# Kernel optimization log

Measured on AMD Instinct MI355X. Metric: run time of the kernel, lower is better.

Reference implementation:

```python
import jax, jax.numpy as jnp
import numpy as np

HID = 512
VOCAB = 2048
K_CB = 4


def conv1d(x, w, b, stride):
    # x: [B, C_in, L], w: [C_out, C_in, 7], torch Conv1d(k=7, stride, pad=3)
    y = jax.lax.conv_general_dilated(
        x, w, window_strides=(stride,), padding=[(3, 3)],
        dimension_numbers=("NCH", "OIH", "NCH"))
    return y + b[None, :, None]


def setup_inputs() -> dict:
    key = jax.random.key(0)
    ks = jax.random.split(key, 9)
    B, S = 4, 32768
    audio = jax.random.normal(ks[0], (B, 1, S), dtype=jnp.float32)
    # encoder params (fan-in scaled init, like torch default scale-wise)
    w1 = jax.random.normal(ks[1], (HID // 4, 1, 7), dtype=jnp.float32) * (1.0 / np.sqrt(1 * 7))
    b1 = jnp.zeros((HID // 4,), dtype=jnp.float32)
    w2 = jax.random.normal(ks[2], (HID // 2, HID // 4, 7), dtype=jnp.float32) * (1.0 / np.sqrt(HID // 4 * 7))
    b2 = jnp.zeros((HID // 2,), dtype=jnp.float32)
    w3 = jax.random.normal(ks[3], (HID, HID // 2, 7), dtype=jnp.float32) * (1.0 / np.sqrt(HID // 2 * 7))
    b3 = jnp.zeros((HID,), dtype=jnp.float32)
    codebook = jax.random.normal(ks[4], (K_CB, VOCAB, HID), dtype=jnp.float32)
    embedding = jax.random.normal(ks[5], (VOCAB, HID), dtype=jnp.float32)
    return {"audio": audio, "w1": w1, "b1": b1, "w2": w2, "b2": b2,
            "w3": w3, "b3": b3, "codebook": codebook, "embedding": embedding}


def reference(audio, w1, b1, w2, b2, w3, b3, codebook, embedding):
    # conv encoder: [B,1,S] -> [B,H,L], L = S/8
    f = jax.nn.relu(conv1d(audio, w1, b1, 2))
    f = jax.nn.relu(conv1d(f, w2, b2, 2))
    f = conv1d(f, w3, b3, 2)
    feats = jnp.transpose(f, (0, 2, 1))  # [B, L, H]

    # multi-codebook nearest neighbor: argmin of squared L2 == argmin of cdist
    f2 = jnp.sum(feats * feats, axis=-1)          # [B, L]
    c2 = jnp.sum(codebook * codebook, axis=-1)    # [K, V]
    cross = jnp.einsum("blh,kvh->bklv", feats, codebook)  # [B, K, L, V]
    d2 = f2[:, None, :, None] + c2[None, :, None, :] - 2.0 * cross
    tokens = jnp.argmin(d2, axis=-1)              # [B, K, L] (stack over codebooks at dim=1)
    emb = embedding[tokens].mean(axis=1)          # [B, L, H]
    return tokens, emb
```

## Files before the change

kernel.cpp:

```cpp
#include <hip/hip_runtime.h>
#include <hip/hip_bf16.h>
#include <stdint.h>

#define B_ 4
#define S_IN 32768
#define C1V 128
#define L1V 16384
#define C2V 256
#define L2V 8192
#define C3V 512
#define L3V 4096
#define VOCABV 2048
#define KCB 4

#define R1P (2 * (L1V + 16))
#define P1P (L1V + 16)
#define R2P (2 * (L2V + 16))
#define P2P (L2V + 16)

typedef _Float16 half8 __attribute__((ext_vector_type(8)));
typedef float floatx4 __attribute__((ext_vector_type(4)));

#define AS1 __attribute__((address_space(1)))
#define AS3 __attribute__((address_space(3)))

__device__ __forceinline__ void gload_lds16(const void* g, void* l) {
    __builtin_amdgcn_global_load_lds((const AS1 void*)g, (AS3 void*)l, 16, 0, 0);
}

__device__ __forceinline__ half8 lds_read_half8_a4(const _Float16* p) {
    union { uint32_t u[4]; half8 h; } t;
    const uint32_t* w = (const uint32_t*)p;
    t.u[0] = w[0]; t.u[1] = w[1]; t.u[2] = w[2]; t.u[3] = w[3];
    return t.h;
}

__global__ void padzero_kernel(_Float16* __restrict__ x1h, _Float16* __restrict__ x2h) {
    int j = blockIdx.x * 256 + threadIdx.x;
    half8 z;
#pragma unroll
    for (int i = 0; i < 8; ++i) z[i] = (_Float16)0.f;
    if (j < 2048) {
        int row = j >> 2, p = j & 3;
        size_t base = (size_t)row * R1P + (size_t)(p >> 1) * P1P + ((p & 1) ? (L1V + 8) : 0);
        *(half8*)(x1h + base) = z;
    } else if (j < 6144) {
        int j2 = j - 2048;
        int row = j2 >> 2, p = j2 & 3;
        size_t base = (size_t)row * R2P + (size_t)(p >> 1) * P2P + ((p & 1) ? (L2V + 8) : 0);
        *(half8*)(x2h + base) = z;
    }
}

__global__ void conv1_kernel(const float* __restrict__ x, const float* __restrict__ w,
                             const float* __restrict__ bias, _Float16* __restrict__ out) {
    __shared__ float xs[2 * 256 + 6];
    __shared__ float ws[7];
    const int l0 = blockIdx.x * 256;
    const int co = blockIdx.y;
    const int b  = blockIdx.z;
    const int tid = threadIdx.x;
    const float* xb = x + (size_t)b * S_IN;
    for (int n = tid; n < 2 * 256 + 6; n += 256) {
        int p = 2 * l0 - 3 + n;
        xs[n] = (p >= 0 && p < S_IN) ? xb[p] : 0.f;
    }
    if (tid < 7) ws[tid] = w[co * 7 + tid];
    __syncthreads();
    float acc = bias[co];
    const int base = 2 * tid;
#pragma unroll
    for (int t = 0; t < 7; ++t) acc = fmaf(ws[t], xs[base + t], acc);
    float s = fmaxf(acc, 0.f) * 1024.f;
    _Float16 h  = (_Float16)s;
    _Float16 lo = (_Float16)(s - (float)h);
    size_t o = (size_t)(b * C1V + co) * R1P + 8 + l0 + tid;
    out[o] = h;
    out[o + P1P] = lo;
}

__global__ void wsplit_kernel(const float* __restrict__ w, _Float16* __restrict__ wh,
                              _Float16* __restrict__ wl, int cin, int cout) {
    int idx = blockIdx.x * 256 + threadIdx.x;
    if (idx >= cin * cout) return;
    int co = idx / cin;
    int ci = idx - co * cin;
    const float* src = w + ((size_t)co * cin + ci) * 7;
    half8 h, l;
    h[0] = (_Float16)0.f; l[0] = (_Float16)0.f;
#pragma unroll
    for (int u = 1; u < 8; ++u) {
        float v = src[u - 1] * 1024.f;
        _Float16 hh = (_Float16)v;
        h[u] = hh;
        l[u] = (_Float16)(v - (float)hh);
    }
    size_t o = (size_t)co * (cin * 8) + ci * 8;
    *(half8*)(wh + o) = h;
    *(half8*)(wl + o) = l;
}


__global__ __launch_bounds__(256, 2) void conv2_mfma_kernel(
    const _Float16* __restrict__ xin, const _Float16* __restrict__ WH,
    const _Float16* __restrict__ WL, const float* __restrict__ bias,
    _Float16* __restrict__ xout) {
    __shared__ _Float16 Xs[2176];
    __shared__ _Float16 WsH[128 * 32], WsL[128 * 32];
    const int tid = threadIdx.x;
    const int wave = tid >> 6;
    const int lane = tid & 63;
    const int wm = wave >> 1, wn = wave & 1;
    const int q  = lane >> 4;
    const int cl = lane & 15;
    const int l0  = blockIdx.x * 128;
    const int co0 = blockIdx.y * 128;
    const int b   = blockIdx.z;

    const int wrow  = lane >> 2;
    const int wseg  = lane & 3;
    const int wsoff = (wseg ^ ((wrow >> 1) & 3)) * 8;
    const int rq    = (q ^ ((cl >> 1) & 3)) * 8;

    const int pl0 = (tid >= 136) ? 1 : 0;
    const int r0  = tid - pl0 * 136;
    const int ci0 = r0 / 34;
    const int sg0 = r0 - ci0 * 34;
    const _Float16* xb = xin + (size_t)b * C1V * R1P;

    floatx4 acc[4][4];
#pragma unroll
    for (int a = 0; a < 4; ++a)
#pragma unroll
        for (int n = 0; n < 4; ++n) acc[a][n] = (floatx4){0.f, 0.f, 0.f, 0.f};

    for (int ch = 0; ch < 32; ++ch) {
        __syncthreads();
        {
            const _Float16* gx = xb + (size_t)(ch * 4 + ci0) * R1P + pl0 * P1P + 2 * l0 + sg0 * 8;
            gload_lds16(gx, (char*)Xs + (tid & ~63) * 16);
            if (tid < 16) {
                const _Float16* gt = xb + (size_t)(ch * 4 + 3) * R1P + P1P + 2 * l0 + (18 + tid) * 8;
                gload_lds16(gt, (char*)Xs + 4096);
            }
        }
        const int k0 = ch * 32;
        for (int g = wave; g < 8; g += 4) {
            const _Float16* gh = WH + (size_t)(co0 + g * 16 + wrow) * 1024 + k0 + wsoff;
            const _Float16* gl = WL + (size_t)(co0 + g * 16 + wrow) * 1024 + k0 + wsoff;
            gload_lds16(gh, (char*)WsH + g * 1024);
            gload_lds16(gl, (char*)WsL + g * 1024);
        }
        asm volatile("s_waitcnt vmcnt(0)" ::: "memory");
        __syncthreads();

        half8 awh[4], awl[4], bxh[4], bxl[4];
#pragma unroll
        for (int a = 0; a < 4; ++a) {
            const int ro = (wm * 64 + a * 16 + cl) * 32 + rq;
            awh[a] = *(const half8*)&WsH[ro];
            awl[a] = *(const half8*)&WsL[ro];
        }
#pragma unroll
        for (int n = 0; n < 4; ++n) {
            const int lrel = wn * 64 + n * 16 + cl;
            bxh[n] = lds_read_half8_a4(&Xs[q * 272 + 4 + 2 * lrel]);
            bxl[n] = lds_read_half8_a4(&Xs[1088 + q * 272 + 4 + 2 * lrel]);
        }
#pragma unroll
        for (int a = 0; a < 4; ++a)
#pragma unroll
            for (int n = 0; n < 4; ++n) {
                acc[a][n] = __builtin_amdgcn_mfma_f32_16x16x32_f16(awh[a], bxh[n], acc[a][n], 0, 0, 0);
                acc[a][n] = __builtin_amdgcn_mfma_f32_16x16x32_f16(awl[a], bxh[n], acc[a][n], 0, 0, 0);
                acc[a][n] = __builtin_amdgcn_mfma_f32_16x16x32_f16(awh[a], bxl[n], acc[a][n], 0, 0, 0);
            }
    }

    float bv[4][4];
#pragma unroll
    for (int a = 0; a < 4; ++a)
#pragma unroll
        for (int r = 0; r < 4; ++r) bv[a][r] = bias[co0 + wm * 64 + a * 16 + q * 4 + r];
#pragma unroll
    for (int a = 0; a < 4; ++a)
#pragma unroll
        for (int n = 0; n < 4; ++n) {
            const int l = l0 + wn * 64 + n * 16 + cl;
#pragma unroll
            for (int r = 0; r < 4; ++r) {
                const int co = co0 + wm * 64 + a * 16 + q * 4 + r;
                float vv = fmaxf(acc[a][n][r] * (1.f / 1048576.f) + bv[a][r], 0.f);
                float s = vv * 1024.f;
                _Float16 h  = (_Float16)s;
                _Float16 lo = (_Float16)(s - (float)h);
                size_t o = (size_t)(b * C2V + co) * R2P + 8 + l;
                xout[o] = h;
                xout[o + P2P] = lo;
            }
        }
}

__global__ __launch_bounds__(256, 2) void conv3_mfma_kernel(
    const _Float16* __restrict__ xin, const _Float16* __restrict__ WH,
    const _Float16* __restrict__ WL, const float* __restrict__ bias,
    _Float16* __restrict__ outh) {
    __shared__ _Float16 Xs[2176];
    __shared__ _Float16 WsH[128 * 32], WsL[128 * 32];
    const int tid = threadIdx.x;
    const int wave = tid >> 6;
    const int lane = tid & 63;
    const int wm = wave >> 1, wn = wave & 1;
    const int q  = lane >> 4;
    const int cl = lane & 15;
    const int l0  = blockIdx.x * 128;
    const int co0 = blockIdx.y * 128;
    const int b   = blockIdx.z;

    const int wrow  = lane >> 2;
    const int wseg  = lane & 3;
    const int wsoff = (wseg ^ ((wrow >> 1) & 3)) * 8;
    const int rq    = (q ^ ((cl >> 1) & 3)) * 8;

    const int pl0 = (tid >= 136) ? 1 : 0;
    const int r0  = tid - pl0 * 136;
    const int ci0 = r0 / 34;
    const int sg0 = r0 - ci0 * 34;
    const _Float16* xb = xin + (size_t)b * C2V * R2P;

    floatx4 acc[4][4];
#pragma unroll
    for (int a = 0; a < 4; ++a)
#pragma unroll
        for (int n = 0; n < 4; ++n) acc[a][n] = (floatx4){0.f, 0.f, 0.f, 0.f};

    for (int ch = 0; ch < 64; ++ch) {
        __syncthreads();
        {
            const _Float16* gx = xb + (size_t)(ch * 4 + ci0) * R2P + pl0 * P2P + 2 * l0 + sg0 * 8;
            gload_lds16(gx, (char*)Xs + (tid & ~63) * 16);
            if (tid < 16) {
                const _Float16* gt = xb + (size_t)(ch * 4 + 3) * R2P + P2P + 2 * l0 + (18 + tid) * 8;
                gload_lds16(gt, (char*)Xs + 4096);
            }
        }
        const int k0 = ch * 32;
        for (int g = wave; g < 8; g += 4) {
            const _Float16* gh = WH + (size_t)(co0 + g * 16 + wrow) * 2048 + k0 + wsoff;
            const _Float16* gl = WL + (size_t)(co0 + g * 16 + wrow) * 2048 + k0 + wsoff;
            gload_lds16(gh, (char*)WsH + g * 1024);
            gload_lds16(gl, (char*)WsL + g * 1024);
        }
        asm volatile("s_waitcnt vmcnt(0)" ::: "memory");
        __syncthreads();

        half8 axh[4], axl[4], bwh[4], bwl[4];
#pragma unroll
        for (int a = 0; a < 4; ++a) {
            const int lrel = wm * 64 + a * 16 + cl;
            axh[a] = lds_read_half8_a4(&Xs[q * 272 + 4 + 2 * lrel]);
            axl[a] = lds_read_half8_a4(&Xs[1088 + q * 272 + 4 + 2 * lrel]);
        }
#pragma unroll
        for (int n = 0; n < 4; ++n) {
            const int ro = (wn * 64 + n * 16 + cl) * 32 + rq;
            bwh[n] = *(const half8*)&WsH[ro];
            bwl[n] = *(const half8*)&WsL[ro];
        }
#pragma unroll
        for (int a = 0; a < 4; ++a)
#pragma unroll
            for (int n = 0; n < 4; ++n) {
                acc[a][n] = __builtin_amdgcn_mfma_f32_16x16x32_f16(axh[a], bwh[n], acc[a][n], 0, 0, 0);
                acc[a][n] = __builtin_amdgcn_mfma_f32_16x16x32_f16(axl[a], bwh[n], acc[a][n], 0, 0, 0);
                acc[a][n] = __builtin_amdgcn_mfma_f32_16x16x32_f16(axh[a], bwl[n], acc[a][n], 0, 0, 0);
            }
    }

    float bv[4];
#pragma unroll
    for (int n = 0; n < 4; ++n) bv[n] = bias[co0 + wn * 64 + n * 16 + cl];
#pragma unroll
    for (int a = 0; a < 4; ++a)
#pragma unroll
        for (int n = 0; n < 4; ++n) {
            const int co = co0 + wn * 64 + n * 16 + cl;
#pragma unroll
            for (int r = 0; r < 4; ++r) {
                const int l = l0 + wm * 64 + a * 16 + q * 4 + r;
                float f = acc[a][n][r] * (1.f / 1048576.f) + bv[n];
                float s = f * 1024.f;
                _Float16 h = (_Float16)s;
                _Float16 lo = (_Float16)(s - (float)h);
                _Float16* dst = outh + ((size_t)b * L3V + l) * 1024 + co;
                dst[0] = h;
                dst[512] = lo;
            }
        }
}

__global__ void cbprep_kernel(const float* __restrict__ cb, _Float16* __restrict__ y,
                              float* __restrict__ c2p) {
    const int r = blockIdx.x;
    const int lane = threadIdx.x;
    const float* row = cb + (size_t)r * 512;
    float4 a = *(const float4*)&row[lane * 8];
    float4 c = *(const float4*)&row[lane * 8 + 4];
    float s = a.x * a.x + a.y * a.y + a.z * a.z + a.w * a.w
            + c.x * c.x + c.y * c.y + c.z * c.z + c.w * c.w;
#pragma unroll
    for (int off = 32; off > 0; off >>= 1) s += __shfl_down(s, off, 64);
    if (lane == 0) c2p[r] = s * 524288.f;

    const float e[8] = {a.x, a.y, a.z, a.w, c.x, c.y, c.z, c.w};
    half8 hv, lv;
#pragma unroll
    for (int i = 0; i < 8; ++i) {
        float v = e[i] * 1024.f;
        _Float16 h = (_Float16)v;
        hv[i] = h;
        lv[i] = (_Float16)(v - (float)h);
    }
    *(half8*)(y + (size_t)r * 1024 + lane * 8) = hv;
    *(half8*)(y + (size_t)r * 1024 + 512 + lane * 8) = lv;
}

__global__ __launch_bounds__(512, 2) void cross_mfma_kernel(
    const _Float16* __restrict__ Af, const _Float16* __restrict__ Bf,
    const float* __restrict__ c2p,
    int* __restrict__ tok_i, float* __restrict__ tok_f) {

    __shared__ _Float16 AsH[2][8192], AsL[2][8192];
    __shared__ _Float16 BsH[2][8192], BsL[2][8192];
    __shared__ float c2s[2048];
    __shared__ float slotv[2][256];
    __shared__ int   sloti[2][256];

    const int tid  = threadIdx.x;
    const int w    = tid >> 6;
    const int lane = tid & 63;
    const int wm = w >> 1;
    const int wn = w & 1;
    const int q  = lane >> 4;
    const int cl = lane & 15;

    const int l0 = blockIdx.x * 256;
    const int k  = blockIdx.y;
    const int b  = blockIdx.z;

    const _Float16* Ab = Af + (size_t)(b * L3V + l0) * 1024;
    const _Float16* Bb = Bf + (size_t)k * VOCABV * 1024;

    {
        float4 cv = *(const float4*)&c2p[k * VOCABV + tid * 4];
        *(float4*)&c2s[tid * 4] = cv;
    }
    if (tid < 256) {
        slotv[0][tid] = -3.4e38f; slotv[1][tid] = -3.4e38f;
        sloti[0][tid] = 0;        sloti[1][tid] = 0;
    }

    const int arow  = w * 16 + (lane >> 2);
    const int bg    = (w >> 1) & 1;
    const int bj    = (w & 1) * 16 + (lane >> 2);
    const int bpl   = w >> 2;
    const int sswz8 = ((lane & 3) ^ ((lane >> 3) & 3)) * 8;
    const int brq   = (q ^ ((cl >> 1) & 3)) * 8;

#define STAGE_A(NXT, KON, PL, H) do { \
    const _Float16* s_ = Ab + (size_t)((H) * 128 + arow) * 1024 + (PL) * 512 + (KON) + sswz8; \
    gload_lds16(s_, ((PL) ? (char*)&AsL[NXT][0] : (char*)&AsH[NXT][0]) \
                     + (H) * 8192 + w * 1024 + lane * 16); \
} while (0)
#define STAGE_B(NXT, VTN, KON, C) do { \
    const _Float16* s_ = Bb + (size_t)((VTN) * 256 + 128 * bg + 32 * (C) + bj) * 1024 \
                         + bpl * 512 + (KON) + sswz8; \
    gload_lds16(s_, (bpl ? (char*)&BsL[NXT][0] : (char*)&BsH[NXT][0]) \
                     + (C) * 4096 + (w & 3) * 1024 + lane * 16); \
} while (0)

#define READ_B(P, H0, L0, H1, L1) do { \
    const int bro_ = (P) * 2048 + wn * 1024 + cl * 32 + brq; \
    H0 = *(const half8*)&BsH[cur][bro_]; \
    L0 = *(const half8*)&BsL[cur][bro_]; \
    H1 = *(const half8*)&BsH[cur][bro_ + 512]; \
    L1 = *(const half8*)&BsL[cur][bro_ + 512]; \
} while (0)

#define MFMA_CHUNK(P, H0, L0, H1, L1) do { \
    __builtin_amdgcn_s_setprio(1); \
    _Pragma("unroll") \
    for (int mt = 0; mt < 4; ++mt) { \
        acc[mt][2*(P)]   = __builtin_amdgcn_mfma_f32_16x16x32_f16(ah[mt], H0, acc[mt][2*(P)], 0, 0, 0); \
        acc[mt][2*(P)]   = __builtin_amdgcn_mfma_f32_16x16x32_f16(al[mt], H0, acc[mt][2*(P)], 0, 0, 0); \
        acc[mt][2*(P)]   = __builtin_amdgcn_mfma_f32_16x16x32_f16(ah[mt], L0, acc[mt][2*(P)], 0, 0, 0); \
        acc[mt][2*(P)+1] = __builtin_amdgcn_mfma_f32_16x16x32_f16(ah[mt], H1, acc[mt][2*(P)+1], 0, 0, 0); \
        acc[mt][2*(P)+1] = __builtin_amdgcn_mfma_f32_16x16x32_f16(al[mt], H1, acc[mt][2*(P)+1], 0, 0, 0); \
        acc[mt][2*(P)+1] = __builtin_amdgcn_mfma_f32_16x16x32_f16(ah[mt], L1, acc[mt][2*(P)+1], 0, 0, 0); \
    } \
    __builtin_amdgcn_s_setprio(0); \
    __builtin_amdgcn_sched_barrier(0); \
} while (0)

    floatx4 acc[4][8];
    half8 ah[4], al[4];
    int cur = 0;

    STAGE_A(0, 0, 0, 0); STAGE_A(0, 0, 0, 1);
    STAGE_A(0, 0, 1, 0); STAGE_A(0, 0, 1, 1);
    STAGE_B(0, 0, 0, 0); STAGE_B(0, 0, 0, 1);
    STAGE_B(0, 0, 0, 2); STAGE_B(0, 0, 0, 3);

#pragma unroll 1
    for (int t = 0; t < 128; ++t) {
        const int nxt = cur ^ 1;
        const int tn  = t + 1;
        const int vtn = tn >> 4;
        const int kon = (tn & 15) << 5;
        const int vt  = t >> 4;

        if ((t & 15) == 0) {
#pragma unroll
            for (int mt = 0; mt < 4; ++mt)
#pragma unroll
                for (int nt = 0; nt < 8; ++nt) acc[mt][nt] = (floatx4){0.f, 0.f, 0.f, 0.f};
        }

        asm volatile("s_waitcnt vmcnt(0)" ::: "memory");
        __builtin_amdgcn_s_barrier();

        half8 s0h0, s0l0, s0h1, s0l1, s1h0, s1l0, s1h1, s1l1;

#pragma unroll
        for (int mt = 0; mt < 4; ++mt) {
            const int aro = (wm * 64 + mt * 16 + cl) * 32 + brq;
            ah[mt] = *(const half8*)&AsH[cur][aro];
            al[mt] = *(const half8*)&AsL[cur][aro];
        }
        READ_B(0, s0h0, s0l0, s0h1, s0l1);
        if (t < 127) { STAGE_A(nxt, kon, 0, 0); STAGE_A(nxt, kon, 0, 1); }
        asm volatile("s_waitcnt lgkmcnt(0)" ::: "memory");
        __builtin_amdgcn_sched_barrier(0);
        MFMA_CHUNK(0, s0h0, s0l0, s0h1, s0l1);
        READ_B(1, s1h0, s1l0, s1h1, s1l1);
        if (t < 127) { STAGE_A(nxt, kon, 1, 0); STAGE_A(nxt, kon, 1, 1); }
        __builtin_amdgcn_sched_barrier(0);

        __builtin_amdgcn_s_barrier();
        asm volatile("s_waitcnt lgkmcnt(0)" ::: "memory");
        __builtin_amdgcn_sched_barrier(0);
        MFMA_CHUNK(1, s1h0, s1l0, s1h1, s1l1);
        READ_B(2, s0h0, s0l0, s0h1, s0l1);
        if (t < 127) { STAGE_B(nxt, vtn, kon, 0); STAGE_B(nxt, vtn, kon, 1); }
        __builtin_amdgcn_sched_barrier(0);

        __builtin_amdgcn_s_barrier();
        asm volatile("s_waitcnt lgkmcnt(0)" ::: "memory");
        __builtin_amdgcn_sched_barrier(0);
        MFMA_CHUNK(2, s0h0, s0l0, s0h1, s0l1);
        READ_B(3, s1h0, s1l0, s1h1, s1l1);
        if (t < 127) { STAGE_B(nxt, vtn, kon, 2); STAGE_B(nxt, vtn, kon, 3); }
        __builtin_amdgcn_sched_barrier(0);

        __builtin_amdgcn_s_barrier();
        asm volatile("s_waitcnt lgkmcnt(0)" ::: "memory");
        __builtin_amdgcn_sched_barrier(0);
        MFMA_CHUNK(3, s1h0, s1l0, s1h1, s1l1);
        cur = nxt;

        if ((t & 15) == 15) {
            float c2v[8];
#pragma unroll
            for (int nt = 0; nt < 8; ++nt)
                c2v[nt] = c2s[vt * 256 + wn * 128 + nt * 16 + cl];
#pragma unroll
            for (int mt = 0; mt < 4; ++mt)
#pragma unroll
                for (int r = 0; r < 4; ++r) {
                    float bv = acc[mt][0][r] - c2v[0];
                    int   bi = vt * 256 + wn * 128 + cl;
#pragma unroll
                    for (int nt = 1; nt < 8; ++nt) {
                        float m = acc[mt][nt][r] - c2v[nt];
                        int   vi = vt * 256 + wn * 128 + nt * 16 + cl;
                        if (m > bv) { bv = m; bi = vi; }
                    }
#pragma unroll
                    for (int msk = 1; msk < 16; msk <<= 1) {
                        float ov = __shfl_xor(bv, msk, 64);
                        int   oi = __shfl_xor(bi, msk, 64);
                        if (ov > bv || (ov == bv && oi < bi)) { bv = ov; bi = oi; }
                    }
                    if (cl == 0) {
                        const int row = wm * 64 + mt * 16 + q * 4 + r;
                        float cur_v = slotv[wn][row];
                        int   ci  = sloti[wn][row];
                        if (bv > cur_v || (bv == cur_v && bi < ci)) {
                            slotv[wn][row] = bv;
                            sloti[wn][row] = bi;
                        }
                    }
                }
        }
    }
#undef MFMA_CHUNK
#undef READ_B
#undef STAGE_A
#undef STAGE_B

    __syncthreads();
    if (tid < 256) {
        float v0 = slotv[0][tid], v1 = slotv[1][tid];
        int   i0 = sloti[0][tid], i1 = sloti[1][tid];
        bool t1 = (v1 > v0);
        int best = t1 ? i1 : i0;
        const int n = (b * KCB + k) * L3V + l0 + tid;
        tok_i[n] = best;
        tok_f[n] = (float)best;
    }
}

__global__ void emb_kernel(const int* __restrict__ tokens, const float* __restrict__ E,
                           float* __restrict__ out) {
    const int l = blockIdx.x;
    const int b = blockIdx.y;
    const int h4 = threadIdx.x * 4;
    const int t0 = tokens[((size_t)(b * KCB + 0)) * L3V + l];
    const int t1 = tokens[((size_t)(b * KCB + 1)) * L3V + l];
    const int t2 = tokens[((size_t)(b * KCB + 2)) * L3V + l];
    const int t3 = tokens[((size_t)(b * KCB + 3)) * L3V + l];
    const float4 e0 = *(const float4*)&E[(size_t)t0 * 512 + h4];
    const float4 e1 = *(const float4*)&E[(size_t)t1 * 512 + h4];
    const float4 e2 = *(const float4*)&E[(size_t)t2 * 512 + h4];
    const float4 e3 = *(const float4*)&E[(size_t)t3 * 512 + h4];
    float4 r;
    r.x = (e0.x + e1.x + e2.x + e3.x) * 0.25f;
    r.y = (e0.y + e1.y + e2.y + e3.y) * 0.25f;
    r.z = (e0.z + e1.z + e2.z + e3.z) * 0.25f;
    r.w = (e0.w + e1.w + e2.w + e3.w) * 0.25f;
    *(float4*)&out[((size_t)b * L3V + l) * 512 + h4] = r;
}

extern "C" void kernel_launch(void* const* d_in, const int* in_sizes, int n_in,
                              void* d_out, int out_size, void* d_ws, size_t ws_size,
                              hipStream_t stream) {
    const float* audio = (const float*)d_in[0];
    const float* w1 = (const float*)d_in[1];
    const float* b1 = (const float*)d_in[2];
    const float* w2 = (const float*)d_in[3];
    const float* b2 = (const float*)d_in[4];
    const float* w3 = (const float*)d_in[5];
    const float* b3 = (const float*)d_in[6];
    const float* cb = (const float*)d_in[7];
    const float* E  = (const float*)d_in[8];

    float* out_tok = (float*)d_out;
    float* out_emb = out_tok + (size_t)B_ * KCB * L3V;

    float* ws = (float*)d_ws;
    size_t off = 0;
    float* x1f = ws + off; off += (size_t)B_ * C1V * (L1V + 16);
    float* x2f = ws + off; off += (size_t)B_ * C2V * (L2V + 16);
    float* w2h_f = ws + off; off += (size_t)C2V * (C1V * 8) / 2;
    float* w2l_f = ws + off; off += (size_t)C2V * (C1V * 8) / 2;
    float* w3h_f = ws + off; off += (size_t)C3V * (C2V * 8) / 2;
    float* w3l_f = ws + off; off += (size_t)C3V * (C2V * 8) / 2;
    float* c2p = ws + off; off += (size_t)KCB * VOCABV;
    int*   tok = (int*)(ws + off); off += (size_t)B_ * KCB * L3V;

    _Float16* X1  = (_Float16*)x1f;
    _Float16* X2  = (_Float16*)x2f;
    _Float16* Afh = (_Float16*)x1f;
    _Float16* Bfh = (_Float16*)x2f;
    _Float16* W2H = (_Float16*)w2h_f; _Float16* W2L = (_Float16*)w2l_f;
    _Float16* W3H = (_Float16*)w3h_f; _Float16* W3L = (_Float16*)w3l_f;

    padzero_kernel<<<24, 256, 0, stream>>>(X1, X2);

    wsplit_kernel<<<(C2V * C1V + 255) / 256, 256, 0, stream>>>(w2, W2H, W2L, C1V, C2V);
    wsplit_kernel<<<(C3V * C2V + 255) / 256, 256, 0, stream>>>(w3, W3H, W3L, C2V, C3V);

    conv1_kernel<<<dim3(L1V / 256, C1V, B_), 256, 0, stream>>>(audio, w1, b1, X1);

    conv2_mfma_kernel<<<dim3(L2V / 128, C2V / 128, B_), 256, 0, stream>>>(
        X1, W2H, W2L, b2, X2);

    conv3_mfma_kernel<<<dim3(L3V / 128, C3V / 128, B_), 256, 0, stream>>>(
        X2, W3H, W3L, b3, Afh);

    cbprep_kernel<<<KCB * VOCABV, 64, 0, stream>>>(cb, Bfh, c2p);

    cross_mfma_kernel<<<dim3(L3V / 256, KCB, B_), 512, 0, stream>>>(
        Afh, Bfh, c2p, tok, out_tok);

    emb_kernel<<<dim3(L3V, B_), 128, 0, stream>>>(tok, E, out_emb);
}
```

Baseline: 609.4 us.

## Switch cross-distance GEMM from 16x16x32 to 32x32x16 MFMA tiles

Recasts the codebook distance GEMM to use 32x32x16 MFMA instructions instead of 16x16x32, which changes the accumulator layout to 2x4 floatx16 tiles, the LDS fragment reads and swizzle, and the argmin epilogue row mapping and shuffle reduction. Larger MFMA tiles raise the arithmetic done per LDS fragment read and reduce the number of B-operand loads. The cost is a longer shuffle reduction in the epilogue (5 steps over 32 lanes) and different register pressure.

```diff
diff --git a/kernel.cpp b/kernel.cpp
--- a/kernel.cpp
+++ b/kernel.cpp
@@ -20,6 +20,7 @@
 
 typedef _Float16 half8 __attribute__((ext_vector_type(8)));
 typedef float floatx4 __attribute__((ext_vector_type(4)));
+typedef float floatx16 __attribute__((ext_vector_type(16)));
 
 #define AS1 __attribute__((address_space(1)))
 #define AS3 __attribute__((address_space(3)))
@@ -99,7 +100,6 @@
     *(half8*)(wh + o) = h;
     *(half8*)(wl + o) = l;
 }
-
 
 __global__ __launch_bounds__(256, 2) void conv2_mfma_kernel(
     const _Float16* __restrict__ xin, const _Float16* __restrict__ WH,
@@ -341,8 +341,8 @@
     const int lane = tid & 63;
     const int wm = w >> 1;
     const int wn = w & 1;
-    const int q  = lane >> 4;
-    const int cl = lane & 15;
+    const int g    = lane >> 5;
+    const int cl32 = lane & 31;
 
     const int l0 = blockIdx.x * 256;
     const int k  = blockIdx.y;
@@ -365,7 +365,7 @@
     const int bj    = (w & 1) * 16 + (lane >> 2);
     const int bpl   = w >> 2;
     const int sswz8 = ((lane & 3) ^ ((lane >> 3) & 3)) * 8;
-    const int brq   = (q ^ ((cl >> 1) & 3)) * 8;
+    const int oK0   = (g ^ ((cl32 >> 1) & 3)) * 8;
 
 #define STAGE_A(NXT, KON, PL, H) do { \
     const _Float16* s_ = Ab + (size_t)((H) * 128 + arow) * 1024 + (PL) * 512 + (KON) + sswz8; \
@@ -379,31 +379,29 @@
                      + (C) * 4096 + (w & 3) * 1024 + lane * 16); \
 } while (0)
 
-#define READ_B(P, H0, L0, H1, L1) do { \
-    const int bro_ = (P) * 2048 + wn * 1024 + cl * 32 + brq; \
-    H0 = *(const half8*)&BsH[cur][bro_]; \
-    L0 = *(const half8*)&BsL[cur][bro_]; \
-    H1 = *(const half8*)&BsH[cur][bro_ + 512]; \
-    L1 = *(const half8*)&BsL[cur][bro_ + 512]; \
+#define READ_B32(NT, KS, H, L) do { \
+    const int bro_ = ((NT) * 64 + wn * 32 + cl32) * 32 + (oK0 ^ ((KS) * 16)); \
+    H = *(const half8*)&BsH[cur][bro_]; \
+    L = *(const half8*)&BsL[cur][bro_]; \
 } while (0)
 
-#define MFMA_CHUNK(P, H0, L0, H1, L1) do { \
+#define MFMA_P(KS, NT0, NT1, BH0, BL0, BH1, BL1) do { \
     __builtin_amdgcn_s_setprio(1); \
     _Pragma("unroll") \
-    for (int mt = 0; mt < 4; ++mt) { \
-        acc[mt][2*(P)]   = __builtin_amdgcn_mfma_f32_16x16x32_f16(ah[mt], H0, acc[mt][2*(P)], 0, 0, 0); \
-        acc[mt][2*(P)]   = __builtin_amdgcn_mfma_f32_16x16x32_f16(al[mt], H0, acc[mt][2*(P)], 0, 0, 0); \
-        acc[mt][2*(P)]   = __builtin_amdgcn_mfma_f32_16x16x32_f16(ah[mt], L0, acc[mt][2*(P)], 0, 0, 0); \
-        acc[mt][2*(P)+1] = __builtin_amdgcn_mfma_f32_16x16x32_f16(ah[mt], H1, acc[mt][2*(P)+1], 0, 0, 0); \
-        acc[mt][2*(P)+1] = __builtin_amdgcn_mfma_f32_16x16x32_f16(al[mt], H1, acc[mt][2*(P)+1], 0, 0, 0); \
-        acc[mt][2*(P)+1] = __builtin_amdgcn_mfma_f32_16x16x32_f16(ah[mt], L1, acc[mt][2*(P)+1], 0, 0, 0); \
+    for (int mt = 0; mt < 2; ++mt) { \
+        acc[mt][NT0] = __builtin_amdgcn_mfma_f32_32x32x16_f16(ah[mt][KS], BH0, acc[mt][NT0], 0, 0, 0); \
+        acc[mt][NT1] = __builtin_amdgcn_mfma_f32_32x32x16_f16(ah[mt][KS], BH1, acc[mt][NT1], 0, 0, 0); \
+        acc[mt][NT0] = __builtin_amdgcn_mfma_f32_32x32x16_f16(al[mt][KS], BH0, acc[mt][NT0], 0, 0, 0); \
+        acc[mt][NT1] = __builtin_amdgcn_mfma_f32_32x32x16_f16(al[mt][KS], BH1, acc[mt][NT1], 0, 0, 0); \
+        acc[mt][NT0] = __builtin_amdgcn_mfma_f32_32x32x16_f16(ah[mt][KS], BL0, acc[mt][NT0], 0, 0, 0); \
+        acc[mt][NT1] = __builtin_amdgcn_mfma_f32_32x32x16_f16(ah[mt][KS], BL1, acc[mt][NT1], 0, 0, 0); \
     } \
     __builtin_amdgcn_s_setprio(0); \
     __builtin_amdgcn_sched_barrier(0); \
 } while (0)
 
-    floatx4 acc[4][8];
-    half8 ah[4], al[4];
+    floatx16 acc[2][4];
+    half8 ah[2][2], al[2][2];
     int cur = 0;
 
     STAGE_A(0, 0, 0, 0); STAGE_A(0, 0, 0, 1);
@@ -421,9 +419,11 @@
 
         if ((t & 15) == 0) {
 #pragma unroll
-            for (int mt = 0; mt < 4; ++mt)
-#pragma unroll
-                for (int nt = 0; nt < 8; ++nt) acc[mt][nt] = (floatx4){0.f, 0.f, 0.f, 0.f};
+            for (int mt = 0; mt < 2; ++mt)
+#pragma unroll
+                for (int nt = 0; nt < 4; ++nt)
+#pragma unroll
+                    for (int r = 0; r < 16; ++r) acc[mt][nt][r] = 0.f;
         }
 
         asm volatile("s_waitcnt vmcnt(0)" ::: "memory");
@@ -432,67 +432,73 @@
         half8 s0h0, s0l0, s0h1, s0l1, s1h0, s1l0, s1h1, s1l1;
 
 #pragma unroll
-        for (int mt = 0; mt < 4; ++mt) {
-            const int aro = (wm * 64 + mt * 16 + cl) * 32 + brq;
-            ah[mt] = *(const half8*)&AsH[cur][aro];
-            al[mt] = *(const half8*)&AsL[cur][aro];
-        }
-        READ_B(0, s0h0, s0l0, s0h1, s0l1);
+        for (int mt = 0; mt < 2; ++mt)
+#pragma unroll
+            for (int ks = 0; ks < 2; ++ks) {
+                const int aro = (wm * 64 + mt * 32 + cl32) * 32 + (oK0 ^ (ks * 16));
+                ah[mt][ks] = *(const half8*)&AsH[cur][aro];
+                al[mt][ks] = *(const half8*)&AsL[cur][aro];
+            }
+        READ_B32(0, 0, s0h0, s0l0);
+        READ_B32(1, 0, s0h1, s0l1);
         if (t < 127) { STAGE_A(nxt, kon, 0, 0); STAGE_A(nxt, kon, 0, 1); }
         asm volatile("s_waitcnt lgkmcnt(0)" ::: "memory");
         __builtin_amdgcn_sched_barrier(0);
-        MFMA_CHUNK(0, s0h0, s0l0, s0h1, s0l1);
-        READ_B(1, s1h0, s1l0, s1h1, s1l1);
+        MFMA_P(0, 0, 1, s0h0, s0l0, s0h1, s0l1);
+        READ_B32(2, 0, s1h0, s1l0);
+        READ_B32(3, 0, s1h1, s1l1);
         if (t < 127) { STAGE_A(nxt, kon, 1, 0); STAGE_A(nxt, kon, 1, 1); }
         __builtin_amdgcn_sched_barrier(0);
 
         __builtin_amdgcn_s_barrier();
         asm volatile("s_waitcnt lgkmcnt(0)" ::: "memory");
         __builtin_amdgcn_sched_barrier(0);
-        MFMA_CHUNK(1, s1h0, s1l0, s1h1, s1l1);
-        READ_B(2, s0h0, s0l0, s0h1, s0l1);
+        MFMA_P(0, 2, 3, s1h0, s1l0, s1h1, s1l1);
+        READ_B32(0, 1, s0h0, s0l0);
+        READ_B32(1, 1, s0h1, s0l1);
         if (t < 127) { STAGE_B(nxt, vtn, kon, 0); STAGE_B(nxt, vtn, kon, 1); }
         __builtin_amdgcn_sched_barrier(0);
 
         __builtin_amdgcn_s_barrier();
         asm volatile("s_waitcnt lgkmcnt(0)" ::: "memory");
         __builtin_amdgcn_sched_barrier(0);
-        MFMA_CHUNK(2, s0h0, s0l0, s0h1, s0l1);
-        READ_B(3, s1h0, s1l0, s1h1, s1l1);
+        MFMA_P(1, 0, 1, s0h0, s0l0, s0h1, s0l1);
+        READ_B32(2, 1, s1h0, s1l0);
+        READ_B32(3, 1, s1h1, s1l1);
         if (t < 127) { STAGE_B(nxt, vtn, kon, 2); STAGE_B(nxt, vtn, kon, 3); }
         __builtin_amdgcn_sched_barrier(0);
 
         __builtin_amdgcn_s_barrier();
         asm volatile("s_waitcnt lgkmcnt(0)" ::: "memory");
         __builtin_amdgcn_sched_barrier(0);
-        MFMA_CHUNK(3, s1h0, s1l0, s1h1, s1l1);
+        MFMA_P(1, 2, 3, s1h0, s1l0, s1h1, s1l1);
         cur = nxt;
 
         if ((t & 15) == 15) {
-            float c2v[8];
-#pragma unroll
-            for (int nt = 0; nt < 8; ++nt)
-                c2v[nt] = c2s[vt * 256 + wn * 128 + nt * 16 + cl];
-#pragma unroll
-            for (int mt = 0; mt < 4; ++mt)
-#pragma unroll
-                for (int r = 0; r < 4; ++r) {
+            float c2v[4];
+#pragma unroll
+            for (int nt = 0; nt < 4; ++nt)
+                c2v[nt] = c2s[vt * 256 + wn * 128 + nt * 32 + cl32];
+#pragma unroll
+            for (int mt = 0; mt < 2; ++mt)
+#pragma unroll
+                for (int r = 0; r < 16; ++r) {
                     float bv = acc[mt][0][r] - c2v[0];
-                    int   bi = vt * 256 + wn * 128 + cl;
-#pragma unroll
-                    for (int nt = 1; nt < 8; ++nt) {
+                    int   bi = vt * 256 + wn * 128 + cl32;
+#pragma unroll
+                    for (int nt = 1; nt < 4; ++nt) {
                         float m = acc[mt][nt][r] - c2v[nt];
-                        int   vi = vt * 256 + wn * 128 + nt * 16 + cl;
+                        int   vi = vt * 256 + wn * 128 + nt * 32 + cl32;
                         if (m > bv) { bv = m; bi = vi; }
                     }
 #pragma unroll
-                    for (int msk = 1; msk < 16; msk <<= 1) {
+                    for (int msk = 1; msk < 32; msk <<= 1) {
                         float ov = __shfl_xor(bv, msk, 64);
                         int   oi = __shfl_xor(bi, msk, 64);
                         if (ov > bv || (ov == bv && oi < bi)) { bv = ov; bi = oi; }
                     }
-                    if (cl == 0) {
-                        const int row = wm * 64 + mt * 16 + q * 4 + r;
+                    if (cl32 == 0) {
+                        const int row = wm * 64 + mt * 32 + (r & 3) + 8 * (r >> 2) + 4 * g;
                         float cur_v = slotv[wn][row];
                         int   ci  = sloti[wn][row];
                         if (bv > cur_v || (bv == cur_v && bi < ci)) {
@@ -503,8 +509,8 @@
                 }
         }
     }
-#undef MFMA_CHUNK
-#undef READ_B
+#undef MFMA_P
+#undef READ_B32
 #undef STAGE_A
 #undef STAGE_B
 
```

Measured after the change: 737.4 us. 1.21x slower.
